# Kernel tuning notes

Measured on AMD Instinct MI355X. Metric: run time of the kernel, lower is better.

Reference implementation:

```python
import jax, jax.numpy as jnp
import numpy as np

IN_F, HID, OUT_F, N_HEADS, BATCH = 256, 512, 2048, 8, 4096


def _kaiming_uniform(key, shape, fan_in):
    # kaiming_uniform_ with a=sqrt(5): gain = sqrt(2/(1+5)) = 1/sqrt(3)
    gain = 1.0 / np.sqrt(3.0)
    bound = gain * np.sqrt(3.0 / fan_in)  # = sqrt(1/fan_in)
    return jax.random.uniform(key, shape, jnp.float32, -bound, bound)


def setup_inputs() -> dict:
    key = jax.random.key(0)
    kx, ki, k1, k2, k3, k4 = jax.random.split(key, 6)
    X = jax.random.normal(kx, (BATCH, IN_F), jnp.float32)
    X_head_idx = jax.random.randint(ki, (BATCH,), 0, N_HEADS)
    # layer 1: in -> hidden
    W1 = _kaiming_uniform(k1, (N_HEADS, IN_F, HID), IN_F)
    b1 = jax.random.uniform(k2, (N_HEADS, HID), jnp.float32,
                            -1.0 / np.sqrt(IN_F), 1.0 / np.sqrt(IN_F))
    # layer 2: hidden -> out
    W2 = _kaiming_uniform(k3, (N_HEADS, HID, OUT_F), HID)
    b2 = jax.random.uniform(k4, (N_HEADS, OUT_F), jnp.float32,
                            -1.0 / np.sqrt(HID), 1.0 / np.sqrt(HID))
    return {"X": X, "X_head_idx": X_head_idx, "W1": W1, "b1": b1,
            "W2": W2, "b2": b2}


def _selective_linear(x, idx, W, b):
    # x: [B, in], W: [H, in, out], b: [H, out], idx: [B]
    # compute all heads densely, then select each sample's head
    y = jnp.einsum('bi,hio->bho', x, W) + b[None]   # [B, H, out]
    return jnp.take_along_axis(y, idx[:, None, None], axis=1)[:, 0, :]


def reference(X, X_head_idx, W1, b1, W2, b2):
    h = _selective_linear(X, X_head_idx, W1, b1)
    h = jax.nn.relu(h)
    out = _selective_linear(h, X_head_idx, W2, b2)
    return out
```

## Files before the change

### kernel.cpp

```cpp
#include <hip/hip_runtime.h>

#define IN_F 256
#define HID 512
#define OUT_F 2048
#define N_HEADS 8
#define BATCH 4096

typedef __bf16 bf16_t;
typedef bf16_t bf16x8 __attribute__((ext_vector_type(8)));
typedef float f32x4 __attribute__((ext_vector_type(4)));

typedef __attribute__((address_space(1))) const unsigned int gu32;
typedef __attribute__((address_space(3))) unsigned int lu32;

__device__ inline unsigned short f2bf(float f) {
  union { float f; unsigned u; } v; v.f = f;
  unsigned u = v.u;
  unsigned r = (u + 0x7FFFu + ((u >> 16) & 1u)) >> 16;
  return (unsigned short)r;
}

__global__ __launch_bounds__(1024) void bucket_kernel(const int* __restrict__ idx,
                                                      int* __restrict__ order,
                                                      int* __restrict__ offsets) {
  __shared__ int cnt[N_HEADS];
  __shared__ int base[N_HEADS + 1];
  __shared__ int cur[N_HEADS];
  int tid = threadIdx.x;
  if (tid < N_HEADS) cnt[tid] = 0;
  __syncthreads();
  for (int i = tid; i < BATCH; i += 1024) atomicAdd(&cnt[idx[i]], 1);
  __syncthreads();
  if (tid == 0) {
    int acc = 0;
    for (int h = 0; h < N_HEADS; ++h) { base[h] = acc; cur[h] = acc; acc += cnt[h]; }
    base[N_HEADS] = acc;
  }
  __syncthreads();
  if (tid < N_HEADS + 1) offsets[tid] = base[tid];
  for (int i = tid; i < BATCH; i += 1024) {
    int pos = atomicAdd(&cur[idx[i]], 1);
    order[pos] = i;
  }
}

__device__ inline void transpose64(const float* __restrict__ W,
                                   unsigned short* __restrict__ Wt,
                                   int K, int N, int b, int nt, int kt,
                                   float (*tile)[65]) {
  int per_head = nt * kt;
  int h = b / per_head;
  int rem = b % per_head;
  int n0 = (rem % nt) * 64;
  int k0 = (rem / nt) * 64;
  const float* Wh = W + (size_t)h * K * N;
  unsigned short* Wth = Wt + (size_t)h * K * N;
  int c = threadIdx.x & 63;
  int r0 = threadIdx.x >> 6;
  for (int rr = r0; rr < 64; rr += 4)
    tile[rr][c] = Wh[(size_t)(k0 + rr) * N + n0 + c];
  __syncthreads();
  for (int rr = r0; rr < 64; rr += 4)
    Wth[(size_t)(n0 + rr) * K + k0 + c] = f2bf(tile[c][rr]);
}

__global__ __launch_bounds__(256) void prep_kernel(const float* __restrict__ X,
                                                   const int* __restrict__ order,
                                                   unsigned short* __restrict__ Xg,
                                                   const float* __restrict__ W1,
                                                   unsigned short* __restrict__ W1t,
                                                   const float* __restrict__ W2,
                                                   unsigned short* __restrict__ W2t) {
  __shared__ float tile[64][65];
  int b = blockIdx.x;
  if (b < 512) {
    int c4 = threadIdx.x & 63;
    int rloc = threadIdx.x >> 6;
#pragma unroll
    for (int pass = 0; pass < 2; ++pass) {
      int p = b * 8 + pass * 4 + rloc;
      int src = order[p];
      float4 v = ((const float4*)(X + (size_t)src * IN_F))[c4];
      ushort4 o;
      o.x = f2bf(v.x); o.y = f2bf(v.y); o.z = f2bf(v.z); o.w = f2bf(v.w);
      ((ushort4*)(Xg + (size_t)p * IN_F))[c4] = o;
    }
  } else if (b < 768) {
    transpose64(W1, W1t, IN_F, HID, b - 512, HID / 64, IN_F / 64, tile);
  } else {
    transpose64(W2, W2t, HID, OUT_F, b - 768, OUT_F / 64, HID / 64, tile);
  }
}

template <int K, int NTOT, int EPI>
__global__ __launch_bounds__(256) void gemm128_kernel(const unsigned short* __restrict__ A,
                                                      const unsigned short* __restrict__ Wt,
                                                      const float* __restrict__ bias,
                                                      const int* __restrict__ offsets,
                                                      const int* __restrict__ order,
                                                      unsigned short* __restrict__ Hout,
                                                      float* __restrict__ Out) {
  constexpr int BM = 128, BN = 128, BK = 32;
  __shared__ __align__(16) unsigned short As[BM * BK];
  __shared__ __align__(16) unsigned short Bs[BN * BK];

  int my = blockIdx.y;
  int head = -1, row0 = 0, rows = 0, acc_t = 0;
#pragma unroll
  for (int h = 0; h < N_HEADS; ++h) {
    int o0 = offsets[h], o1 = offsets[h + 1];
    int cnt = o1 - o0;
    int t = (cnt + BM - 1) / BM;
    if (head < 0 && my < acc_t + t) {
      head = h;
      int lt = my - acc_t;
      row0 = o0 + lt * BM;
      rows = min(BM, cnt - lt * BM);
    }
    acc_t += t;
  }
  if (head < 0) return;

  int n0 = blockIdx.x * BN;
  const unsigned short* Bh = Wt + (size_t)head * (size_t)NTOT * K;

  int tid = threadIdx.x;
  int wave = tid >> 6;
  int lane = tid & 63;
  int q = lane >> 4;
  int l16 = lane & 15;

  int ldrow = lane >> 2;
  int ldcol = (lane & 3) * 8;
  int c0 = wave * 2, c1 = wave * 2 + 1;
  int ar0 = row0 + min(c0 * 16 + ldrow, rows - 1);
  int ar1 = row0 + min(c1 * 16 + ldrow, rows - 1);
  const unsigned short* aptr0 = A + (size_t)ar0 * K + ldcol;
  const unsigned short* aptr1 = A + (size_t)ar1 * K + ldcol;
  const unsigned short* bptr0 = Bh + (size_t)(n0 + c0 * 16 + ldrow) * K + ldcol;
  const unsigned short* bptr1 = Bh + (size_t)(n0 + c1 * 16 + ldrow) * K + ldcol;
  unsigned short* lA0 = As + c0 * 512;
  unsigned short* lA1 = As + c1 * 512;
  unsigned short* lB0 = Bs + c0 * 512;
  unsigned short* lB1 = Bs + c1 * 512;

  int w_m = wave >> 1, w_n = wave & 1;

  f32x4 acc[4][4];
#pragma unroll
  for (int i = 0; i < 4; ++i)
#pragma unroll
    for (int j = 0; j < 4; ++j) acc[i][j] = (f32x4){0.f, 0.f, 0.f, 0.f};

  for (int k0 = 0; k0 < K; k0 += BK) {
    __builtin_amdgcn_global_load_lds((gu32*)aptr0, (lu32*)lA0, 16, 0, 0);
    __builtin_amdgcn_global_load_lds((gu32*)aptr1, (lu32*)lA1, 16, 0, 0);
    __builtin_amdgcn_global_load_lds((gu32*)bptr0, (lu32*)lB0, 16, 0, 0);
    __builtin_amdgcn_global_load_lds((gu32*)bptr1, (lu32*)lB1, 16, 0, 0);
    aptr0 += BK; aptr1 += BK; bptr0 += BK; bptr1 += BK;
    __syncthreads();

    bf16x8 af[4], bfr[4];
#pragma unroll
    for (int i = 0; i < 4; ++i) {
      af[i] = *(const bf16x8*)(As + (w_m * 64 + i * 16 + l16) * BK + q * 8);
      bfr[i] = *(const bf16x8*)(Bs + (w_n * 64 + i * 16 + l16) * BK + q * 8);
    }
#pragma unroll
    for (int mi = 0; mi < 4; ++mi)
#pragma unroll
      for (int ni = 0; ni < 4; ++ni)
        acc[mi][ni] = __builtin_amdgcn_mfma_f32_16x16x32_bf16(af[mi], bfr[ni], acc[mi][ni], 0, 0, 0);
    __syncthreads();
  }

  float bval[4];
#pragma unroll
  for (int ni = 0; ni < 4; ++ni)
    bval[ni] = bias[(size_t)head * NTOT + n0 + w_n * 64 + ni * 16 + l16];

#pragma unroll
  for (int mi = 0; mi < 4; ++mi) {
#pragma unroll
    for (int r = 0; r < 4; ++r) {
      int m = w_m * 64 + mi * 16 + q * 4 + r;
      if (m < rows) {
        int p = row0 + m;
        if (EPI == 0) {
#pragma unroll
          for (int ni = 0; ni < 4; ++ni) {
            int n = n0 + w_n * 64 + ni * 16 + l16;
            float v = acc[mi][ni][r] + bval[ni];
            v = v > 0.f ? v : 0.f;
            Hout[(size_t)p * NTOT + n] = f2bf(v);
          }
        } else {
          int rg = order[p];
#pragma unroll
          for (int ni = 0; ni < 4; ++ni) {
            int n = n0 + w_n * 64 + ni * 16 + l16;
            Out[(size_t)rg * NTOT + n] = acc[mi][ni][r] + bval[ni];
          }
        }
      }
    }
  }
}

extern "C" void kernel_launch(void* const* d_in, const int* in_sizes, int n_in,
                              void* d_out, int out_size, void* d_ws, size_t ws_size,
                              hipStream_t stream) {
  const float* X = (const float*)d_in[0];
  const int* idxh = (const int*)d_in[1];
  const float* W1 = (const float*)d_in[2];
  const float* b1 = (const float*)d_in[3];
  const float* W2 = (const float*)d_in[4];
  const float* b2 = (const float*)d_in[5];
  float* out = (float*)d_out;

  char* ws = (char*)d_ws;
  int* order = (int*)ws;                     ws += (size_t)BATCH * 4;
  int* offsets = (int*)ws;                   ws += 64;
  unsigned short* Xg = (unsigned short*)ws;  ws += (size_t)BATCH * IN_F * 2;
  unsigned short* W1t = (unsigned short*)ws; ws += (size_t)N_HEADS * IN_F * HID * 2;
  unsigned short* W2t = (unsigned short*)ws; ws += (size_t)N_HEADS * HID * OUT_F * 2;
  unsigned short* Hb = (unsigned short*)ws;  ws += (size_t)BATCH * HID * 2;

  bucket_kernel<<<dim3(1), dim3(1024), 0, stream>>>(idxh, order, offsets);
  prep_kernel<<<dim3(2816), dim3(256), 0, stream>>>(X, order, Xg, W1, W1t, W2, W2t);

  constexpr int MT = BATCH / 128 + N_HEADS;
  gemm128_kernel<IN_F, HID, 0><<<dim3(HID / 128, MT), dim3(256), 0, stream>>>(
      Xg, W1t, b1, offsets, order, Hb, nullptr);
  gemm128_kernel<HID, OUT_F, 1><<<dim3(OUT_F / 128, MT), dim3(256), 0, stream>>>(
      Hb, W2t, b2, offsets, order, nullptr, out);
}
```

Baseline: 132.0 us.

## Fuse bucket, weight transpose and both GEMMs into one cooperative persistent kernel

Replaces four kernel launches with a single cooperative persistent kernel. It runs bucketing and weight transposition, then grid-syncs, runs GEMM1, grid-syncs again and runs GEMM2 over a strided tile loop. The X gather and bf16 conversion move into GEMM1's A-tile load, which removes the Xg intermediate buffer and its pass. The goal is to cut launch gaps and an extra memory pass, at the cost of grid-sync overhead and a grid limited to 512 persistent blocks. The old multi-kernel path stays as a fallback if the cooperative launch fails.

```diff
diff --git a/kernel.cpp b/kernel.cpp
--- a/kernel.cpp
+++ b/kernel.cpp
@@ -1,10 +1,14 @@
 #include <hip/hip_runtime.h>
+#include <hip/hip_cooperative_groups.h>
+
+namespace cg = cooperative_groups;
 
 #define IN_F 256
 #define HID 512
 #define OUT_F 2048
 #define N_HEADS 8
 #define BATCH 4096
+#define MT 40
 
 typedef __bf16 bf16_t;
 typedef bf16_t bf16x8 __attribute__((ext_vector_type(8)));
@@ -20,191 +24,312 @@
   return (unsigned short)r;
 }
 
-__global__ __launch_bounds__(1024) void bucket_kernel(const int* __restrict__ idx,
-                                                      int* __restrict__ order,
-                                                      int* __restrict__ offsets) {
-  __shared__ int cnt[N_HEADS];
-  __shared__ int base[N_HEADS + 1];
-  __shared__ int cur[N_HEADS];
-  int tid = threadIdx.x;
+__device__ __forceinline__ bool map_tile(const int* offsets, int my,
+                                         int& head, int& row0, int& rows) {
+  head = -1;
+  int acc_t = 0;
+#pragma unroll
+  for (int h = 0; h < N_HEADS; ++h) {
+    int o0 = offsets[h], o1 = offsets[h + 1];
+    int cnt = o1 - o0;
+    int t = (cnt + 127) >> 7;
+    if (head < 0 && my < acc_t + t) {
+      head = h;
+      int lt = my - acc_t;
+      row0 = o0 + lt * 128;
+      rows = min(128, cnt - lt * 128);
+    }
+    acc_t += t;
+  }
+  return head >= 0;
+}
+
+
+__device__ __forceinline__ void bucket_body(const int* __restrict__ idxh,
+                                            int* __restrict__ order,
+                                            int* __restrict__ offsets,
+                                            char* smem, int tid) {
+  int* cnt = (int*)smem;
+  int* basep = cnt + 8;
+  int* cur = basep + 9;
   if (tid < N_HEADS) cnt[tid] = 0;
   __syncthreads();
-  for (int i = tid; i < BATCH; i += 1024) atomicAdd(&cnt[idx[i]], 1);
+  for (int i = tid; i < BATCH; i += 256) atomicAdd(&cnt[idxh[i]], 1);
   __syncthreads();
   if (tid == 0) {
-    int acc = 0;
-    for (int h = 0; h < N_HEADS; ++h) { base[h] = acc; cur[h] = acc; acc += cnt[h]; }
-    base[N_HEADS] = acc;
-  }
-  __syncthreads();
-  if (tid < N_HEADS + 1) offsets[tid] = base[tid];
-  for (int i = tid; i < BATCH; i += 1024) {
-    int pos = atomicAdd(&cur[idx[i]], 1);
+    int a = 0;
+#pragma unroll
+    for (int h = 0; h < N_HEADS; ++h) { basep[h] = a; cur[h] = a; a += cnt[h]; }
+    basep[N_HEADS] = a;
+  }
+  __syncthreads();
+  if (tid < N_HEADS + 1) offsets[tid] = basep[tid];
+  for (int i = tid; i < BATCH; i += 256) {
+    int pos = atomicAdd(&cur[idxh[i]], 1);
     order[pos] = i;
   }
 }
 
-__device__ inline void transpose64(const float* __restrict__ W,
-                                   unsigned short* __restrict__ Wt,
-                                   int K, int N, int b, int nt, int kt,
-                                   float (*tile)[65]) {
+__device__ __forceinline__ void transpose_body(const float* __restrict__ W1,
+                                               unsigned short* __restrict__ W1t,
+                                               const float* __restrict__ W2,
+                                               unsigned short* __restrict__ W2t,
+                                               char* smem, int tid, int t) {
+  float (*tile)[65] = (float(*)[65])smem;
+  int c = tid & 63, r0 = tid >> 6;
+  const float* W; unsigned short* Wt; int K, N, b, nt, kt;
+  if (t < 256) { W = W1; Wt = W1t; K = IN_F; N = HID; b = t; nt = 8; kt = 4; }
+  else { W = W2; Wt = W2t; K = HID; N = OUT_F; b = t - 256; nt = 32; kt = 8; }
   int per_head = nt * kt;
-  int h = b / per_head;
-  int rem = b % per_head;
-  int n0 = (rem % nt) * 64;
-  int k0 = (rem / nt) * 64;
+  int h = b / per_head, rem = b % per_head;
+  int n0 = (rem % nt) * 64, k0 = (rem / nt) * 64;
   const float* Wh = W + (size_t)h * K * N;
   unsigned short* Wth = Wt + (size_t)h * K * N;
-  int c = threadIdx.x & 63;
-  int r0 = threadIdx.x >> 6;
   for (int rr = r0; rr < 64; rr += 4)
     tile[rr][c] = Wh[(size_t)(k0 + rr) * N + n0 + c];
   __syncthreads();
   for (int rr = r0; rr < 64; rr += 4)
     Wth[(size_t)(n0 + rr) * K + k0 + c] = f2bf(tile[c][rr]);
-}
-
-__global__ __launch_bounds__(256) void prep_kernel(const float* __restrict__ X,
-                                                   const int* __restrict__ order,
-                                                   unsigned short* __restrict__ Xg,
+  __syncthreads();
+}
+
+__device__ __forceinline__ void gemm1_tile(const float* __restrict__ X,
+                                           const int* __restrict__ order,
+                                           const unsigned short* __restrict__ W1t,
+                                           const float* __restrict__ b1,
+                                           unsigned short* __restrict__ Hb,
+                                           int head, int row0, int rows, int n0,
+                                           char* smem, int tid) {
+  unsigned short* As = (unsigned short*)smem;
+  unsigned short* Bs = (unsigned short*)(smem + 8192);
+  int wave = tid >> 6, lane = tid & 63;
+  int q = lane >> 4, l16 = lane & 15;
+  int w_m = wave >> 1, w_n = wave & 1;
+  int ldrow = lane >> 2, ldcol = (lane & 3) * 8;
+  int c0 = wave * 2, c1 = c0 + 1;
+  int arow = tid >> 1, acolh = (tid & 1) * 16;
+
+  const unsigned short* Bh = W1t + (size_t)head * HID * IN_F;
+  const unsigned short* bp0 = Bh + (size_t)(n0 + c0 * 16 + ldrow) * IN_F + ldcol;
+  const unsigned short* bp1 = Bh + (size_t)(n0 + c1 * 16 + ldrow) * IN_F + ldcol;
+  unsigned short* lB0 = Bs + c0 * 512;
+  unsigned short* lB1 = Bs + c1 * 512;
+  int src = order[row0 + min(arow, rows - 1)];
+  const float* xrow = X + (size_t)src * IN_F + acolh;
+  unsigned short* aw = As + arow * 32 + acolh;
+
+  f32x4 acc[4][4];
+#pragma unroll
+  for (int i = 0; i < 4; ++i)
+#pragma unroll
+    for (int j = 0; j < 4; ++j) acc[i][j] = (f32x4){0.f, 0.f, 0.f, 0.f};
+
+  for (int k0 = 0; k0 < IN_F; k0 += 32) {
+    __builtin_amdgcn_global_load_lds((gu32*)bp0, (lu32*)lB0, 16, 0, 0);
+    __builtin_amdgcn_global_load_lds((gu32*)bp1, (lu32*)lB1, 16, 0, 0);
+    bp0 += 32; bp1 += 32;
+    const float4* xp = (const float4*)(xrow + k0);
+    float4 f0 = xp[0], f1 = xp[1], f2 = xp[2], f3 = xp[3];
+    uint4 o0, o1;
+    o0.x = (unsigned)f2bf(f0.x) | ((unsigned)f2bf(f0.y) << 16);
+    o0.y = (unsigned)f2bf(f0.z) | ((unsigned)f2bf(f0.w) << 16);
+    o0.z = (unsigned)f2bf(f1.x) | ((unsigned)f2bf(f1.y) << 16);
+    o0.w = (unsigned)f2bf(f1.z) | ((unsigned)f2bf(f1.w) << 16);
+    o1.x = (unsigned)f2bf(f2.x) | ((unsigned)f2bf(f2.y) << 16);
+    o1.y = (unsigned)f2bf(f2.z) | ((unsigned)f2bf(f2.w) << 16);
+    o1.z = (unsigned)f2bf(f3.x) | ((unsigned)f2bf(f3.y) << 16);
+    o1.w = (unsigned)f2bf(f3.z) | ((unsigned)f2bf(f3.w) << 16);
+    *(uint4*)aw = o0;
+    *(uint4*)(aw + 8) = o1;
+    __syncthreads();
+
+    bf16x8 af[4], bfr[4];
+#pragma unroll
+    for (int i = 0; i < 4; ++i) {
+      af[i] = *(const bf16x8*)(As + (w_m * 64 + i * 16 + l16) * 32 + q * 8);
+      bfr[i] = *(const bf16x8*)(Bs + (w_n * 64 + i * 16 + l16) * 32 + q * 8);
+    }
+#pragma unroll
+    for (int mi = 0; mi < 4; ++mi)
+#pragma unroll
+      for (int ni = 0; ni < 4; ++ni)
+        acc[mi][ni] = __builtin_amdgcn_mfma_f32_16x16x32_bf16(af[mi], bfr[ni], acc[mi][ni], 0, 0, 0);
+    __syncthreads();
+  }
+
+  float bval[4];
+#pragma unroll
+  for (int ni = 0; ni < 4; ++ni)
+    bval[ni] = b1[(size_t)head * HID + n0 + w_n * 64 + ni * 16 + l16];
+#pragma unroll
+  for (int mi = 0; mi < 4; ++mi) {
+#pragma unroll
+    for (int r = 0; r < 4; ++r) {
+      int m = w_m * 64 + mi * 16 + q * 4 + r;
+      if (m < rows) {
+        int p = row0 + m;
+#pragma unroll
+        for (int ni = 0; ni < 4; ++ni) {
+          int n = n0 + w_n * 64 + ni * 16 + l16;
+          float v = acc[mi][ni][r] + bval[ni];
+          v = v > 0.f ? v : 0.f;
+          Hb[(size_t)p * HID + n] = f2bf(v);
+        }
+      }
+    }
+  }
+}
+
+__device__ __forceinline__ void gemm2_tile(const unsigned short* __restrict__ Hb,
+                                           const unsigned short* __restrict__ W2t,
+                                           const float* __restrict__ b2,
+                                           const int* __restrict__ order,
+                                           float* __restrict__ out,
+                                           int head, int row0, int rows, int n0,
+                                           char* smem, int tid) {
+  unsigned short* As = (unsigned short*)smem;
+  unsigned short* Bs = (unsigned short*)(smem + 8192);
+  int wave = tid >> 6, lane = tid & 63;
+  int q = lane >> 4, l16 = lane & 15;
+  int w_m = wave >> 1, w_n = wave & 1;
+  int ldrow = lane >> 2, ldcol = (lane & 3) * 8;
+  int c0 = wave * 2, c1 = c0 + 1;
+
+  const unsigned short* Bh = W2t + (size_t)head * (size_t)OUT_F * HID;
+  int ar0 = row0 + min(c0 * 16 + ldrow, rows - 1);
+  int ar1 = row0 + min(c1 * 16 + ldrow, rows - 1);
+  const unsigned short* ap0 = Hb + (size_t)ar0 * HID + ldcol;
+  const unsigned short* ap1 = Hb + (size_t)ar1 * HID + ldcol;
+  const unsigned short* bp0 = Bh + (size_t)(n0 + c0 * 16 + ldrow) * HID + ldcol;
+  const unsigned short* bp1 = Bh + (size_t)(n0 + c1 * 16 + ldrow) * HID + ldcol;
+  unsigned short* lA0 = As + c0 * 512;
+  unsigned short* lA1 = As + c1 * 512;
+  unsigned short* lB0 = Bs + c0 * 512;
+  unsigned short* lB1 = Bs + c1 * 512;
+
+  f32x4 acc[4][4];
+#pragma unroll
+  for (int i = 0; i < 4; ++i)
+#pragma unroll
+    for (int j = 0; j < 4; ++j) acc[i][j] = (f32x4){0.f, 0.f, 0.f, 0.f};
+
+  for (int k0 = 0; k0 < HID; k0 += 32) {
+    __builtin_amdgcn_global_load_lds((gu32*)ap0, (lu32*)lA0, 16, 0, 0);
+    __builtin_amdgcn_global_load_lds((gu32*)ap1, (lu32*)lA1, 16, 0, 0);
+    __builtin_amdgcn_global_load_lds((gu32*)bp0, (lu32*)lB0, 16, 0, 0);
+    __builtin_amdgcn_global_load_lds((gu32*)bp1, (lu32*)lB1, 16, 0, 0);
+    ap0 += 32; ap1 += 32; bp0 += 32; bp1 += 32;
+    __syncthreads();
+
+    bf16x8 af[4], bfr[4];
+#pragma unroll
+    for (int i = 0; i < 4; ++i) {
+      af[i] = *(const bf16x8*)(As + (w_m * 64 + i * 16 + l16) * 32 + q * 8);
+      bfr[i] = *(const bf16x8*)(Bs + (w_n * 64 + i * 16 + l16) * 32 + q * 8);
+    }
+#pragma unroll
+    for (int mi = 0; mi < 4; ++mi)
+#pragma unroll
+      for (int ni = 0; ni < 4; ++ni)
+        acc[mi][ni] = __builtin_amdgcn_mfma_f32_16x16x32_bf16(af[mi], bfr[ni], acc[mi][ni], 0, 0, 0);
+    __syncthreads();
+  }
+
+  float bval[4];
+#pragma unroll
+  for (int ni = 0; ni < 4; ++ni)
+    bval[ni] = b2[(size_t)head * OUT_F + n0 + w_n * 64 + ni * 16 + l16];
+#pragma unroll
+  for (int mi = 0; mi < 4; ++mi) {
+#pragma unroll
+    for (int r = 0; r < 4; ++r) {
+      int m = w_m * 64 + mi * 16 + q * 4 + r;
+      if (m < rows) {
+        int rg = order[row0 + m];
+#pragma unroll
+        for (int ni = 0; ni < 4; ++ni) {
+          int n = n0 + w_n * 64 + ni * 16 + l16;
+          out[(size_t)rg * OUT_F + n] = acc[mi][ni][r] + bval[ni];
+        }
+      }
+    }
+  }
+}
+
+__global__ __launch_bounds__(256, 2) void mega_kernel(
+    const float* __restrict__ X, const int* __restrict__ idxh,
+    const float* __restrict__ W1, const float* __restrict__ b1,
+    const float* __restrict__ W2, const float* __restrict__ b2,
+    float* __restrict__ out,
+    int* order, int* offsets,
+    unsigned short* __restrict__ W1t, unsigned short* __restrict__ W2t,
+    unsigned short* __restrict__ Hb) {
+  __shared__ __align__(16) char smem[16640];
+  cg::grid_group grid = cg::this_grid();
+  int tid = threadIdx.x;
+
+  if (blockIdx.x == 0) {
+    bucket_body(idxh, order, offsets, smem, tid);
+  } else {
+    for (int t = (int)blockIdx.x - 1; t < 2304; t += (int)gridDim.x - 1)
+      transpose_body(W1, W1t, W2, W2t, smem, tid, t);
+  }
+  grid.sync();
+
+  for (int t = blockIdx.x; t < MT * 4; t += gridDim.x) {
+    int my = t >> 2, nx = t & 3;
+    int head, row0, rows;
+    if (!map_tile(offsets, my, head, row0, rows)) continue;
+    gemm1_tile(X, order, W1t, b1, Hb, head, row0, rows, nx * 128, smem, tid);
+  }
+  grid.sync();
+
+  for (int t = blockIdx.x; t < MT * 16; t += gridDim.x) {
+    int my = t >> 4, nx = t & 15;
+    int head, row0, rows;
+    if (!map_tile(offsets, my, head, row0, rows)) continue;
+    gemm2_tile(Hb, W2t, b2, order, out, head, row0, rows, nx * 128, smem, tid);
+  }
+}
+
+__global__ __launch_bounds__(256) void prep_kernel(const int* __restrict__ idxh,
+                                                   int* order, int* offsets,
                                                    const float* __restrict__ W1,
                                                    unsigned short* __restrict__ W1t,
                                                    const float* __restrict__ W2,
                                                    unsigned short* __restrict__ W2t) {
-  __shared__ float tile[64][65];
-  int b = blockIdx.x;
-  if (b < 512) {
-    int c4 = threadIdx.x & 63;
-    int rloc = threadIdx.x >> 6;
-#pragma unroll
-    for (int pass = 0; pass < 2; ++pass) {
-      int p = b * 8 + pass * 4 + rloc;
-      int src = order[p];
-      float4 v = ((const float4*)(X + (size_t)src * IN_F))[c4];
-      ushort4 o;
-      o.x = f2bf(v.x); o.y = f2bf(v.y); o.z = f2bf(v.z); o.w = f2bf(v.w);
-      ((ushort4*)(Xg + (size_t)p * IN_F))[c4] = o;
-    }
-  } else if (b < 768) {
-    transpose64(W1, W1t, IN_F, HID, b - 512, HID / 64, IN_F / 64, tile);
+  __shared__ __align__(16) char smem[16640];
+  int tid = threadIdx.x;
+  if (blockIdx.x == 0) {
+    bucket_body(idxh, order, offsets, smem, tid);
   } else {
-    transpose64(W2, W2t, HID, OUT_F, b - 768, OUT_F / 64, HID / 64, tile);
-  }
-}
-
-template <int K, int NTOT, int EPI>
-__global__ __launch_bounds__(256) void gemm128_kernel(const unsigned short* __restrict__ A,
-                                                      const unsigned short* __restrict__ Wt,
-                                                      const float* __restrict__ bias,
-                                                      const int* __restrict__ offsets,
-                                                      const int* __restrict__ order,
-                                                      unsigned short* __restrict__ Hout,
-                                                      float* __restrict__ Out) {
-  constexpr int BM = 128, BN = 128, BK = 32;
-  __shared__ __align__(16) unsigned short As[BM * BK];
-  __shared__ __align__(16) unsigned short Bs[BN * BK];
-
-  int my = blockIdx.y;
-  int head = -1, row0 = 0, rows = 0, acc_t = 0;
-#pragma unroll
-  for (int h = 0; h < N_HEADS; ++h) {
-    int o0 = offsets[h], o1 = offsets[h + 1];
-    int cnt = o1 - o0;
-    int t = (cnt + BM - 1) / BM;
-    if (head < 0 && my < acc_t + t) {
-      head = h;
-      int lt = my - acc_t;
-      row0 = o0 + lt * BM;
-      rows = min(BM, cnt - lt * BM);
-    }
-    acc_t += t;
-  }
-  if (head < 0) return;
-
-  int n0 = blockIdx.x * BN;
-  const unsigned short* Bh = Wt + (size_t)head * (size_t)NTOT * K;
-
-  int tid = threadIdx.x;
-  int wave = tid >> 6;
-  int lane = tid & 63;
-  int q = lane >> 4;
-  int l16 = lane & 15;
-
-  int ldrow = lane >> 2;
-  int ldcol = (lane & 3) * 8;
-  int c0 = wave * 2, c1 = wave * 2 + 1;
-  int ar0 = row0 + min(c0 * 16 + ldrow, rows - 1);
-  int ar1 = row0 + min(c1 * 16 + ldrow, rows - 1);
-  const unsigned short* aptr0 = A + (size_t)ar0 * K + ldcol;
-  const unsigned short* aptr1 = A + (size_t)ar1 * K + ldcol;
-  const unsigned short* bptr0 = Bh + (size_t)(n0 + c0 * 16 + ldrow) * K + ldcol;
-  const unsigned short* bptr1 = Bh + (size_t)(n0 + c1 * 16 + ldrow) * K + ldcol;
-  unsigned short* lA0 = As + c0 * 512;
-  unsigned short* lA1 = As + c1 * 512;
-  unsigned short* lB0 = Bs + c0 * 512;
-  unsigned short* lB1 = Bs + c1 * 512;
-
-  int w_m = wave >> 1, w_n = wave & 1;
-
-  f32x4 acc[4][4];
-#pragma unroll
-  for (int i = 0; i < 4; ++i)
-#pragma unroll
-    for (int j = 0; j < 4; ++j) acc[i][j] = (f32x4){0.f, 0.f, 0.f, 0.f};
-
-  for (int k0 = 0; k0 < K; k0 += BK) {
-    __builtin_amdgcn_global_load_lds((gu32*)aptr0, (lu32*)lA0, 16, 0, 0);
-    __builtin_amdgcn_global_load_lds((gu32*)aptr1, (lu32*)lA1, 16, 0, 0);
-    __builtin_amdgcn_global_load_lds((gu32*)bptr0, (lu32*)lB0, 16, 0, 0);
-    __builtin_amdgcn_global_load_lds((gu32*)bptr1, (lu32*)lB1, 16, 0, 0);
-    aptr0 += BK; aptr1 += BK; bptr0 += BK; bptr1 += BK;
-    __syncthreads();
-
-    bf16x8 af[4], bfr[4];
-#pragma unroll
-    for (int i = 0; i < 4; ++i) {
-      af[i] = *(const bf16x8*)(As + (w_m * 64 + i * 16 + l16) * BK + q * 8);
-      bfr[i] = *(const bf16x8*)(Bs + (w_n * 64 + i * 16 + l16) * BK + q * 8);
-    }
-#pragma unroll
-    for (int mi = 0; mi < 4; ++mi)
-#pragma unroll
-      for (int ni = 0; ni < 4; ++ni)
-        acc[mi][ni] = __builtin_amdgcn_mfma_f32_16x16x32_bf16(af[mi], bfr[ni], acc[mi][ni], 0, 0, 0);
-    __syncthreads();
-  }
-
-  float bval[4];
-#pragma unroll
-  for (int ni = 0; ni < 4; ++ni)
-    bval[ni] = bias[(size_t)head * NTOT + n0 + w_n * 64 + ni * 16 + l16];
-
-#pragma unroll
-  for (int mi = 0; mi < 4; ++mi) {
-#pragma unroll
-    for (int r = 0; r < 4; ++r) {
-      int m = w_m * 64 + mi * 16 + q * 4 + r;
-      if (m < rows) {
-        int p = row0 + m;
-        if (EPI == 0) {
-#pragma unroll
-          for (int ni = 0; ni < 4; ++ni) {
-            int n = n0 + w_n * 64 + ni * 16 + l16;
-            float v = acc[mi][ni][r] + bval[ni];
-            v = v > 0.f ? v : 0.f;
-            Hout[(size_t)p * NTOT + n] = f2bf(v);
-          }
-        } else {
-          int rg = order[p];
-#pragma unroll
-          for (int ni = 0; ni < 4; ++ni) {
-            int n = n0 + w_n * 64 + ni * 16 + l16;
-            Out[(size_t)rg * NTOT + n] = acc[mi][ni][r] + bval[ni];
-          }
-        }
-      }
-    }
-  }
+    for (int t = (int)blockIdx.x - 1; t < 2304; t += (int)gridDim.x - 1)
+      transpose_body(W1, W1t, W2, W2t, smem, tid, t);
+  }
+}
+
+__global__ __launch_bounds__(256) void gemm1_kernel(const float* __restrict__ X,
+                                                    const int* __restrict__ order,
+                                                    const int* __restrict__ offsets,
+                                                    const unsigned short* __restrict__ W1t,
+                                                    const float* __restrict__ b1,
+                                                    unsigned short* __restrict__ Hb) {
+  __shared__ __align__(16) char smem[16384];
+  int head, row0, rows;
+  if (!map_tile(offsets, blockIdx.y, head, row0, rows)) return;
+  gemm1_tile(X, order, W1t, b1, Hb, head, row0, rows, blockIdx.x * 128, smem, threadIdx.x);
+}
+
+__global__ __launch_bounds__(256) void gemm2_kernel(const unsigned short* __restrict__ Hb,
+                                                    const unsigned short* __restrict__ W2t,
+                                                    const float* __restrict__ b2,
+                                                    const int* __restrict__ offsets,
+                                                    const int* __restrict__ order,
+                                                    float* __restrict__ out) {
+  __shared__ __align__(16) char smem[16384];
+  int head, row0, rows;
+  if (!map_tile(offsets, blockIdx.y, head, row0, rows)) return;
+  gemm2_tile(Hb, W2t, b2, order, out, head, row0, rows, blockIdx.x * 128, smem, threadIdx.x);
 }
 
 extern "C" void kernel_launch(void* const* d_in, const int* in_sizes, int n_in,
@@ -221,17 +346,28 @@
   char* ws = (char*)d_ws;
   int* order = (int*)ws;                     ws += (size_t)BATCH * 4;
   int* offsets = (int*)ws;                   ws += 64;
-  unsigned short* Xg = (unsigned short*)ws;  ws += (size_t)BATCH * IN_F * 2;
   unsigned short* W1t = (unsigned short*)ws; ws += (size_t)N_HEADS * IN_F * HID * 2;
   unsigned short* W2t = (unsigned short*)ws; ws += (size_t)N_HEADS * HID * OUT_F * 2;
   unsigned short* Hb = (unsigned short*)ws;  ws += (size_t)BATCH * HID * 2;
 
-  bucket_kernel<<<dim3(1), dim3(1024), 0, stream>>>(idxh, order, offsets);
-  prep_kernel<<<dim3(2816), dim3(256), 0, stream>>>(X, order, Xg, W1, W1t, W2, W2t);
-
-  constexpr int MT = BATCH / 128 + N_HEADS;
-  gemm128_kernel<IN_F, HID, 0><<<dim3(HID / 128, MT), dim3(256), 0, stream>>>(
-      Xg, W1t, b1, offsets, order, Hb, nullptr);
-  gemm128_kernel<HID, OUT_F, 1><<<dim3(OUT_F / 128, MT), dim3(256), 0, stream>>>(
-      Hb, W2t, b2, offsets, order, nullptr, out);
-}
+  bool coop_ok = false;
+  int nb = 0;
+  if (hipOccupancyMaxActiveBlocksPerMultiprocessor(&nb, (const void*)mega_kernel,
+                                                   256, 0) == hipSuccess && nb >= 1) {
+    int grid = nb * 256;
+    if (grid > 512) grid = 512;
+    void* args[] = {(void*)&X, (void*)&idxh, (void*)&W1, (void*)&b1,
+                    (void*)&W2, (void*)&b2, (void*)&out,
+                    (void*)&order, (void*)&offsets,
+                    (void*)&W1t, (void*)&W2t, (void*)&Hb};
+    if (hipLaunchCooperativeKernel((void*)mega_kernel, dim3(grid), dim3(256),
+                                   (void**)args, 0, stream) == hipSuccess)
+      coop_ok = true;
+  }
+
+  if (!coop_ok) {
+    prep_kernel<<<dim3(512), dim3(256), 0, stream>>>(idxh, order, offsets, W1, W1t, W2, W2t);
+    gemm1_kernel<<<dim3(HID / 128, MT), dim3(256), 0, stream>>>(X, order, offsets, W1t, b1, Hb);
+    gemm2_kernel<<<dim3(OUT_F / 128, MT), dim3(256), 0, stream>>>(Hb, W2t, b2, offsets, order, out);
+  }
+}
```

Measured after the change: 238.2 us. 1.8x slower.
